# Performance work log

Hardware: AMD Instinct MI355X
Metric: run time of the kernel (lower is better)

Reference implementation:

```python
import jax, jax.numpy as jnp
import numpy as np

STATE_LEN = 512
DIM_KEY = 128


def _rope(t, offset):
    # t: (b, h, s, d) -> rotate-half RoPE with given position offset
    b, h, s, d = t.shape
    inv_freq = 1.0 / (10000.0 ** (jnp.arange(0, d, 2, dtype=jnp.float32) / d))
    pos = jnp.arange(s, dtype=jnp.float32) + offset
    ang = pos[:, None] * inv_freq[None, :]            # (s, d/2)
    cos = jnp.concatenate([jnp.cos(ang), jnp.cos(ang)], axis=-1)  # (s, d)
    sin = jnp.concatenate([jnp.sin(ang), jnp.sin(ang)], axis=-1)
    t1, t2 = t[..., : d // 2], t[..., d // 2 :]
    rot = jnp.concatenate([-t2, t1], axis=-1)
    return t * cos + rot * sin


def _proj(x, w):
    # StackedLinear: mixes heads and features. x: (b,h,s,d), w: (h_in,h_out,d_in,d_out)
    return jnp.einsum('bhsd,hgde->bgse', x, w)


def setup_inputs() -> dict:
    key = jax.random.key(0)
    ks = jax.random.split(key, 10)
    x = jax.random.normal(ks[0], (2, 8, 3072, 128), dtype=jnp.float32)
    wshape = (8, 8, 128, 128)
    names = ['Wq', 'Wk', 'Wv', 'Wqs', 'Wks', 'Wvs', 'Wqe', 'Wke', 'Wve']
    inp = {'x': x}
    for i, n in enumerate(names):
        inp[n] = jax.random.normal(ks[i + 1], wshape, dtype=jnp.float32) * 0.02
    inp['offset'] = 0
    return inp


def reference(x, Wq, Wk, Wv, Wqs, Wks, Wvs, Wqe, Wke, Wve, offset):
    # extract_state: front state, middle, end state along seq axis
    xs = x[:, :, :STATE_LEN]
    xm = x[:, :, STATE_LEN:-STATE_LEN]
    xe = x[:, :, -STATE_LEN:]

    q = jnp.concatenate([_proj(xs, Wqs), _proj(xm, Wq), _proj(xe, Wqe)], axis=2)
    k = jnp.concatenate([_proj(xs, Wks), _proj(xm, Wk), _proj(xe, Wke)], axis=2)
    v = jnp.concatenate([_proj(xs, Wvs), _proj(xm, Wv), _proj(xe, Wve)], axis=2)

    q = _rope(q, offset)
    k = _rope(k, offset)

    scores = jnp.einsum('bhqd,bhkd->bhqk', q, k) / (DIM_KEY ** 0.5)
    s = scores.shape[-1]
    mask = jnp.tril(jnp.ones((s, s), dtype=bool))
    scores = jnp.where(mask[None, None], scores, -jnp.inf)
    att = jax.nn.softmax(scores, axis=-1)
    return jnp.einsum('bhqk,bhkd->bhqd', att, v)
```

## Files before the change

### kernel.cpp

```cpp
#include <hip/hip_runtime.h>
#include <hip/hip_bf16.h>
#include <stdint.h>


typedef __bf16   bf16x8 __attribute__((ext_vector_type(8)));
typedef float    f32x4  __attribute__((ext_vector_type(4)));
typedef uint32_t u32x4  __attribute__((ext_vector_type(4)));
typedef uint16_t u16x4  __attribute__((ext_vector_type(4)));

struct f2 { float c, s; };

#define SEQ   3072
#define NFRQ  64

static __device__ __forceinline__ uint16_t f2bf(float f) {
  union { float f; uint32_t u; } v; v.f = f;
  uint32_t r = (v.u + 0x7FFFu + ((v.u >> 16) & 1u)) >> 16;
  return (uint16_t)r;
}
static __device__ __forceinline__ float bf2f(uint16_t u) {
  union { uint32_t u; float f; } v; v.u = ((uint32_t)u) << 16;
  return v.f;
}
static __device__ __forceinline__ bf16x8 ldlds(const uint16_t* base, int byteoff) {
  u32x4 t = *reinterpret_cast<const u32x4*>(reinterpret_cast<const char*>(base) + byteoff);
  return __builtin_bit_cast(bf16x8, t);
}
static __device__ __forceinline__ bf16x8 ldglb(const uint16_t* p) {
  u32x4 t = *reinterpret_cast<const u32x4*>(p);
  return __builtin_bit_cast(bf16x8, t);
}

__global__ __launch_bounds__(256) void rope_table_kernel(f2* tab, const int* offp) {
  int i = blockIdx.x * 256 + threadIdx.x;
  if (i >= SEQ * NFRQ) return;
  int s = i >> 6, f = i & 63;
  float pos = (float)(s + offp[0]);
  float inv = powf(10000.0f, -(float)(2 * f) / 128.0f);
  float ang = pos * inv;
  tab[i].c = cosf(ang);
  tab[i].s = sinf(ang);
}

__global__ __launch_bounds__(256) void conv_x_kernel(const float* __restrict__ x,
                                                     uint16_t* __restrict__ xb) {
  int i = blockIdx.x * 256 + threadIdx.x;
  int d4 = i & 31;
  int t  = i >> 5;
  int s  = t % 3072;
  int bh = t / 3072;
  int h  = bh & 7, b = bh >> 3;
  f32x4 v = reinterpret_cast<const f32x4*>(x)[i];
  u16x4 o = { f2bf(v[0]), f2bf(v[1]), f2bf(v[2]), f2bf(v[3]) };
  size_t dst = ((size_t)(b * 3072 + s)) * 1024 + h * 128 + d4 * 4;
  *reinterpret_cast<u16x4*>(xb + dst) = o;
}

__global__ __launch_bounds__(256) void trans_w_kernel(
    const float* W0, const float* W1, const float* W2,
    const float* W3, const float* W4, const float* W5,
    const float* W6, const float* W7, const float* W8,
    uint16_t* __restrict__ Wt) {
  const float* Wall[9] = { W0, W1, W2, W3, W4, W5, W6, W7, W8 };
  int blk  = blockIdx.x;
  int widx = blk >> 6;
  int hg   = blk & 63;
  int h = hg >> 3, g = hg & 7;
  int qkv = widx / 3, seg = widx % 3;
  int sel = (seg == 0) ? (3 + qkv) : ((seg == 1) ? qkv : (6 + qkv));
  const float* src = Wall[sel] + (((size_t)h * 8 + g) * 128) * 128;
  uint16_t* dst = Wt + (((size_t)widx * 8 + g) * 128) * 1024 + h * 128;

  __shared__ uint16_t T[128 * 129];
  int tid = threadIdx.x;
  #pragma unroll
  for (int i = 0; i < 16; ++i) {
    int idx = tid + i * 256;
    int d = idx >> 5, e4 = idx & 31;
    f32x4 v = *reinterpret_cast<const f32x4*>(src + d * 128 + e4 * 4);
    int base = d * 129 + e4 * 4;
    T[base + 0] = f2bf(v[0]); T[base + 1] = f2bf(v[1]);
    T[base + 2] = f2bf(v[2]); T[base + 3] = f2bf(v[3]);
  }
  __syncthreads();
  #pragma unroll
  for (int i = 0; i < 8; ++i) {
    int idx = tid + i * 256;
    int e = idx >> 4, c = idx & 15, d0 = c * 8;
    uint32_t w0 = (uint32_t)T[(d0 + 0) * 129 + e] | ((uint32_t)T[(d0 + 1) * 129 + e] << 16);
    uint32_t w1 = (uint32_t)T[(d0 + 2) * 129 + e] | ((uint32_t)T[(d0 + 3) * 129 + e] << 16);
    uint32_t w2 = (uint32_t)T[(d0 + 4) * 129 + e] | ((uint32_t)T[(d0 + 5) * 129 + e] << 16);
    uint32_t w3 = (uint32_t)T[(d0 + 6) * 129 + e] | ((uint32_t)T[(d0 + 7) * 129 + e] << 16);
    u32x4 o = { w0, w1, w2, w3 };
    *reinterpret_cast<u32x4*>(dst + (size_t)e * 1024 + d0) = o;
  }
}

__global__ __launch_bounds__(256) void proj_kernel(
    const uint16_t* __restrict__ xb, const uint16_t* __restrict__ Wt,
    const f2* __restrict__ rtab,
    uint16_t* __restrict__ qb, uint16_t* __restrict__ kb,
    uint16_t* __restrict__ vtb) {
  const int bid = blockIdx.x;
  const int qkv = bid / 384;
  const int rem = bid % 384;
  const int mt  = rem >> 3;
  const int g   = rem & 7;
  const int R0  = mt * 128;
  const int b   = R0 / 3072;
  const int s0  = R0 % 3072;
  const int seg = (s0 < 512) ? 0 : ((s0 < 2560) ? 1 : 2);

  const uint16_t* Ag = xb + (size_t)R0 * 1024;
  const uint16_t* Bg = Wt + (((size_t)(qkv * 3 + seg) * 8 + g) << 17);

  __shared__ __align__(16) uint16_t Al[128 * 64];
  __shared__ __align__(16) uint16_t Bl[128 * 64];

  const int tid  = threadIdx.x;
  const int lane = tid & 63;
  const int w    = tid >> 6;
  const int l15  = lane & 15;
  const int l4   = lane >> 4;

  f32x4 acc[2][8];
  #pragma unroll
  for (int rf = 0; rf < 2; ++rf)
    #pragma unroll
    for (int nf = 0; nf < 8; ++nf) acc[rf][nf] = (f32x4){0.f, 0.f, 0.f, 0.f};

  for (int k0 = 0; k0 < 1024; k0 += 64) {
    #pragma unroll
    for (int i = 0; i < 4; ++i) {
      int idx = tid + i * 256;
      int r = idx >> 3, c8 = idx & 7;
      int off = (r * 128 + c8 * 16) ^ ((r & 7) << 4);
      u32x4 va = *reinterpret_cast<const u32x4*>(Ag + (size_t)r * 1024 + k0 + c8 * 8);
      *reinterpret_cast<u32x4*>(reinterpret_cast<char*>(Al) + off) = va;
      u32x4 vb = *reinterpret_cast<const u32x4*>(Bg + (size_t)r * 1024 + k0 + c8 * 8);
      *reinterpret_cast<u32x4*>(reinterpret_cast<char*>(Bl) + off) = vb;
    }
    __syncthreads();

    bf16x8 af[2][2];
    #pragma unroll
    for (int rf = 0; rf < 2; ++rf)
      #pragma unroll
      for (int kf = 0; kf < 2; ++kf) {
        int row = w * 32 + rf * 16 + l15;
        af[rf][kf] = ldlds(Al, (row * 128 + kf * 64 + l4 * 16) ^ ((row & 7) << 4));
      }
    #pragma unroll
    for (int nf = 0; nf < 8; ++nf) {
      int row = nf * 16 + l15;
      bf16x8 b0 = ldlds(Bl, (row * 128 + 0  + l4 * 16) ^ ((row & 7) << 4));
      bf16x8 b1 = ldlds(Bl, (row * 128 + 64 + l4 * 16) ^ ((row & 7) << 4));
      #pragma unroll
      for (int rf = 0; rf < 2; ++rf) {
        acc[rf][nf] = __builtin_amdgcn_mfma_f32_16x16x32_bf16(af[rf][0], b0, acc[rf][nf], 0, 0, 0);
        acc[rf][nf] = __builtin_amdgcn_mfma_f32_16x16x32_bf16(af[rf][1], b1, acc[rf][nf], 0, 0, 0);
      }
    }
    __syncthreads();
  }

  const int bg = b * 8 + g;
  if (qkv == 2) {
    #pragma unroll
    for (int rf = 0; rf < 2; ++rf)
      #pragma unroll
      for (int nf = 0; nf < 8; ++nf) {
        int e = nf * 16 + l15;
        int s = s0 + w * 32 + rf * 16 + l4 * 4;
        u16x4 pk = { f2bf(acc[rf][nf][0]), f2bf(acc[rf][nf][1]),
                     f2bf(acc[rf][nf][2]), f2bf(acc[rf][nf][3]) };
        *reinterpret_cast<u16x4*>(vtb + ((size_t)bg * 128 + e) * 3072 + s) = pk;
      }
  } else {
    uint16_t* outp = (qkv == 0) ? qb : kb;
    const float scl = (qkv == 0) ? 0.08838834764831845f : 1.0f;
    #pragma unroll
    for (int rf = 0; rf < 2; ++rf)
      #pragma unroll
      for (int j = 0; j < 4; ++j) {
        int s = s0 + w * 32 + rf * 16 + l4 * 4 + j;
        size_t rowb = ((size_t)bg * 3072 + s) * 128;
        #pragma unroll
        for (int nf = 0; nf < 4; ++nf) {
          int f = nf * 16 + l15;
          f2 cs = rtab[s * 64 + f];
          float q1 = acc[rf][nf][j], q2 = acc[rf][nf + 4][j];
          outp[rowb + f]      = f2bf((q1 * cs.c - q2 * cs.s) * scl);
          outp[rowb + 64 + f] = f2bf((q2 * cs.c + q1 * cs.s) * scl);
        }
      }
  }
}

__global__ __launch_bounds__(256) void attn_kernel(
    const uint16_t* __restrict__ qb, const uint16_t* __restrict__ kb,
    const uint16_t* __restrict__ vtb, float* __restrict__ out,
    float* __restrict__ opart, float* __restrict__ lsum) {
  const int bid = blockIdx.x;
  const int bg  = bid & 15;
  const int idx = 47 - (bid >> 4);
  int qt, c;
  if (idx < 8)       { qt = idx;               c = 0; }
  else if (idx < 24) { qt = 8 + ((idx - 8) >> 1);  c = (idx - 8) & 1; }
  else               { int r = idx - 24; qt = 16 + r / 3; c = r - (qt - 16) * 3; }
  const int q0  = qt * 128;
  const int nkv = 2 * qt + 2;
  const int t0  = c * 16;
  const int t1  = (t0 + 16 < nkv) ? (t0 + 16) : nkv;

  const uint16_t* Qp = qb  + (size_t)bg * 3072 * 128;
  const uint16_t* Kp = kb  + (size_t)bg * 3072 * 128;
  const uint16_t* Vp = vtb + (size_t)bg * 128 * 3072;

  __shared__ __align__(16) uint16_t Kl[2][64 * 128];
  __shared__ __align__(16) uint16_t Vl[128 * 64];
  __shared__ __align__(16) uint16_t Pl[128 * 64];

  const int tid  = threadIdx.x;
  const int lane = tid & 63;
  const int w    = tid >> 6;
  const int l15  = lane & 15;
  const int l4   = lane >> 4;
  const int wrow = w * 32;

  bf16x8 aq[2][4];
  #pragma unroll
  for (int rf = 0; rf < 2; ++rf)
    #pragma unroll
    for (int kf = 0; kf < 4; ++kf) {
      int row = q0 + wrow + rf * 16 + l15;
      aq[rf][kf] = ldglb(Qp + (size_t)row * 128 + kf * 32 + l4 * 8);
    }

  f32x4 acc[2][8];
  #pragma unroll
  for (int rf = 0; rf < 2; ++rf)
    #pragma unroll
    for (int ef = 0; ef < 8; ++ef) acc[rf][ef] = (f32x4){0.f, 0.f, 0.f, 0.f};
  float lrow[2][4];
  #pragma unroll
  for (int rf = 0; rf < 2; ++rf)
    #pragma unroll
    for (int j = 0; j < 4; ++j) lrow[rf][j] = 0.f;

  u32x4 kreg[4], vreg[4];
  {
    const int k0 = t0 * 64;
    #pragma unroll
    for (int i = 0; i < 4; ++i) {
      int id2 = tid + i * 256;
      kreg[i] = *reinterpret_cast<const u32x4*>(Kp + (size_t)(k0 + (id2 >> 4)) * 128 + (id2 & 15) * 8);
      vreg[i] = *reinterpret_cast<const u32x4*>(Vp + (size_t)(id2 >> 3) * 3072 + k0 + (id2 & 7) * 8);
    }
    #pragma unroll
    for (int i = 0; i < 4; ++i) {
      int id2 = tid + i * 256;
      int r = id2 >> 4, cc = id2 & 15;
      *reinterpret_cast<u32x4*>(reinterpret_cast<char*>(Kl[0]) +
          ((r * 256 + cc * 16) ^ ((r & 7) << 4))) = kreg[i];
      int e = id2 >> 3, c8 = id2 & 7;
      *reinterpret_cast<u32x4*>(reinterpret_cast<char*>(Vl) +
          ((e * 128 + c8 * 16) ^ ((e & 7) << 4))) = vreg[i];
    }
  }

  for (int t = t0; t < t1; ++t) {
    const int lt = (t - t0) & 1;
    __syncthreads();
    const bool more = (t + 1 < t1);
    if (more) {
      const int k0n = (t + 1) * 64;
      #pragma unroll
      for (int i = 0; i < 4; ++i) {
        int id2 = tid + i * 256;
        kreg[i] = *reinterpret_cast<const u32x4*>(Kp + (size_t)(k0n + (id2 >> 4)) * 128 + (id2 & 15) * 8);
        vreg[i] = *reinterpret_cast<const u32x4*>(Vp + (size_t)(id2 >> 3) * 3072 + k0n + (id2 & 7) * 8);
      }
    }

    const int k0 = t * 64;
    if (k0 <= q0 + wrow + 31) {
      f32x4 sc[2][4];
      #pragma unroll
      for (int rf = 0; rf < 2; ++rf)
        #pragma unroll
        for (int nf = 0; nf < 4; ++nf) sc[rf][nf] = (f32x4){0.f, 0.f, 0.f, 0.f};

      #pragma unroll
      for (int nf = 0; nf < 4; ++nf) {
        int row = nf * 16 + l15;
        #pragma unroll
        for (int kf = 0; kf < 4; ++kf) {
          bf16x8 bk = ldlds(Kl[lt], (row * 256 + kf * 64 + l4 * 16) ^ ((row & 7) << 4));
          #pragma unroll
          for (int rf = 0; rf < 2; ++rf)
            sc[rf][nf] = __builtin_amdgcn_mfma_f32_16x16x32_bf16(aq[rf][kf], bk, sc[rf][nf], 0, 0, 0);
        }
      }

      if (k0 + 63 > q0 + wrow) {
        #pragma unroll
        for (int rf = 0; rf < 2; ++rf)
          #pragma unroll
          for (int nf = 0; nf < 4; ++nf)
            #pragma unroll
            for (int j = 0; j < 4; ++j) {
              int qr = q0 + wrow + rf * 16 + l4 * 4 + j;
              int kc = k0 + nf * 16 + l15;
              if (kc > qr) sc[rf][nf][j] = -1.0e30f;
            }
      }

      #pragma unroll
      for (int rf = 0; rf < 2; ++rf)
        #pragma unroll
        for (int nf = 0; nf < 4; ++nf)
          #pragma unroll
          for (int j = 0; j < 4; ++j) {
            float p  = __expf(sc[rf][nf][j] - 3.0f);
            uint16_t pb = f2bf(p);
            lrow[rf][j] += bf2f(pb);
            int qr = wrow + rf * 16 + l4 * 4 + j;
            int kc = nf * 16 + l15;
            *reinterpret_cast<uint16_t*>(reinterpret_cast<char*>(Pl) +
                ((qr * 128 + kc * 2) ^ ((qr & 7) << 4))) = pb;
          }

      bf16x8 ap[2][2];
      #pragma unroll
      for (int rf = 0; rf < 2; ++rf)
        #pragma unroll
        for (int kf = 0; kf < 2; ++kf) {
          int row = wrow + rf * 16 + l15;
          ap[rf][kf] = ldlds(Pl, (row * 128 + kf * 64 + l4 * 16) ^ ((row & 7) << 4));
        }
      #pragma unroll
      for (int ef = 0; ef < 8; ++ef) {
        int e = ef * 16 + l15;
        bf16x8 bv0 = ldlds(Vl, (e * 128 + 0  + l4 * 16) ^ ((e & 7) << 4));
        bf16x8 bv1 = ldlds(Vl, (e * 128 + 64 + l4 * 16) ^ ((e & 7) << 4));
        #pragma unroll
        for (int rf = 0; rf < 2; ++rf) {
          acc[rf][ef] = __builtin_amdgcn_mfma_f32_16x16x32_bf16(ap[rf][0], bv0, acc[rf][ef], 0, 0, 0);
          acc[rf][ef] = __builtin_amdgcn_mfma_f32_16x16x32_bf16(ap[rf][1], bv1, acc[rf][ef], 0, 0, 0);
        }
      }
    }

    if (more) {
      #pragma unroll
      for (int i = 0; i < 4; ++i) {
        int id2 = tid + i * 256;
        int r = id2 >> 4, cc = id2 & 15;
        *reinterpret_cast<u32x4*>(reinterpret_cast<char*>(Kl[lt ^ 1]) +
            ((r * 256 + cc * 16) ^ ((r & 7) << 4))) = kreg[i];
      }
      __syncthreads();
      #pragma unroll
      for (int i = 0; i < 4; ++i) {
        int id2 = tid + i * 256;
        int e = id2 >> 3, c8 = id2 & 7;
        *reinterpret_cast<u32x4*>(reinterpret_cast<char*>(Vl) +
            ((e * 128 + c8 * 16) ^ ((e & 7) << 4))) = vreg[i];
      }
    }
  }

  const int chunkid = bg * 48 + idx;
  float* obase;
  if (c == 0) {
    obase = out + ((size_t)bg * 3072 + q0) * 128;
  } else {
    int slot = bg * 24 + ((qt < 16) ? (qt - 8) : (8 + (qt - 16) * 2 + (c - 1)));
    obase = opart + (size_t)slot * 16384;
  }
  #pragma unroll
  for (int rf = 0; rf < 2; ++rf)
    #pragma unroll
    for (int j = 0; j < 4; ++j) {
      float ps = lrow[rf][j];
      #pragma unroll
      for (int off = 1; off < 16; off <<= 1)
        ps += __shfl_xor(ps, off);
      int rl = wrow + rf * 16 + l4 * 4 + j;
      if (l15 == 0)
        lsum[(size_t)chunkid * 128 + rl] = ps;
      #pragma unroll
      for (int ef = 0; ef < 8; ++ef)
        obase[(size_t)rl * 128 + ef * 16 + l15] = acc[rf][ef][j];
    }
}

__global__ __launch_bounds__(256) void combine_kernel(
    float* __restrict__ out, const float* __restrict__ opart,
    const float* __restrict__ lsum) {
  const int bid = blockIdx.x;
  const int bg = bid / 24, qt = bid % 24;
  const int nc = (qt < 8) ? 1 : ((qt < 16) ? 2 : 3);
  const int idx0 = (qt < 8) ? qt : ((qt < 16) ? (8 + (qt - 8) * 2) : (24 + (qt - 16) * 3));
  const int t = threadIdx.x;
  const int r = t >> 1, half = t & 1;

  const float* lb = lsum + (size_t)(bg * 48 + idx0) * 128 + r;
  float l = lb[0];
  if (nc > 1) l += lb[128];
  if (nc > 2) l += lb[256];
  float inv = 1.0f / l;

  float* orow = out + ((size_t)bg * 3072 + qt * 128 + r) * 128 + half * 64;
  f32x4 a[16];
  #pragma unroll
  for (int v = 0; v < 16; ++v)
    a[v] = reinterpret_cast<const f32x4*>(orow)[v];
  if (nc > 1) {
    int slot = bg * 24 + ((qt < 16) ? (qt - 8) : (8 + (qt - 16) * 2));
    const float* p = opart + (size_t)slot * 16384 + r * 128 + half * 64;
    #pragma unroll
    for (int v = 0; v < 16; ++v) a[v] += reinterpret_cast<const f32x4*>(p)[v];
  }
  if (nc > 2) {
    int slot = bg * 24 + (8 + (qt - 16) * 2 + 1);
    const float* p = opart + (size_t)slot * 16384 + r * 128 + half * 64;
    #pragma unroll
    for (int v = 0; v < 16; ++v) a[v] += reinterpret_cast<const f32x4*>(p)[v];
  }
  #pragma unroll
  for (int v = 0; v < 16; ++v)
    reinterpret_cast<f32x4*>(orow)[v] = a[v] * inv;
}

extern "C" void kernel_launch(void* const* d_in, const int* in_sizes, int n_in,
                              void* d_out, int out_size, void* d_ws, size_t ws_size,
                              hipStream_t stream) {
  const float* x = (const float*)d_in[0];
  const float* W[9];
  for (int i = 0; i < 9; ++i) W[i] = (const float*)d_in[1 + i];
  const int* offset = (const int*)d_in[10];
  float* out = (float*)d_out;

  char* ws = (char*)d_ws;
  f2*       rtab  = (f2*)(ws + 0);
  uint16_t* xb    = (uint16_t*)(ws + 1572864);
  uint16_t* Wt    = (uint16_t*)(ws + 14155776);
  uint16_t* qb    = (uint16_t*)(ws + 33030144);
  uint16_t* kb    = (uint16_t*)(ws + 45613056);
  uint16_t* vtb   = (uint16_t*)(ws + 58195968);
  float*    opart = (float*)(ws + 0);
  float*    lsum  = (float*)(ws + 25165824);

  hipLaunchKernelGGL(rope_table_kernel, dim3(768),  dim3(256), 0, stream, rtab, offset);
  hipLaunchKernelGGL(conv_x_kernel,     dim3(6144), dim3(256), 0, stream, x, xb);
  hipLaunchKernelGGL(trans_w_kernel,    dim3(576),  dim3(256), 0, stream,
                     W[0], W[1], W[2], W[3], W[4], W[5], W[6], W[7], W[8], Wt);
  hipLaunchKernelGGL(proj_kernel,       dim3(1152), dim3(256), 0, stream,
                     xb, Wt, rtab, qb, kb, vtb);
  hipLaunchKernelGGL(attn_kernel,       dim3(768),  dim3(256), 0, stream,
                     qb, kb, vtb, out, opart, lsum);
  hipLaunchKernelGGL(combine_kernel,    dim3(384),  dim3(256), 0, stream,
                     out, opart, lsum);
}
```

Before: 238.8 us.

## Split attention KV range into finer chunks with table-driven scheduling and bf16 partials

Attention work is split into chunks of 8 KV tiles instead of 16, giving 84 chunks per head instead of 48. Blocks are scheduled through lookup tables so the longest query tiles go first. The QK MFMA operands are swapped so each lane holds a query row, which lets P be written to LDS as packed 8-byte stores and shrinks the row-sum reduction. Partial outputs are now stored as bf16, which halves partial-buffer traffic but adds more partials to combine and some precision loss.

```diff
diff --git a/kernel.cpp b/kernel.cpp
--- a/kernel.cpp
+++ b/kernel.cpp
@@ -6,12 +6,26 @@
 typedef __bf16   bf16x8 __attribute__((ext_vector_type(8)));
 typedef float    f32x4  __attribute__((ext_vector_type(4)));
 typedef uint32_t u32x4  __attribute__((ext_vector_type(4)));
+typedef uint32_t u32x2  __attribute__((ext_vector_type(2)));
 typedef uint16_t u16x4  __attribute__((ext_vector_type(4)));
 
 struct f2 { float c, s; };
 
 #define SEQ   3072
 #define NFRQ  64
+
+__device__ const uint8_t TQT[84] = {
+  3,4,5,6, 7,7,8,8,9,9,10,10, 11,11,11,12,12,12,13,13,13,14,14,14,
+  15,15,15,15,16,16,16,16,17,17,17,17,18,18,18,18,
+  19,19,19,19,19,20,20,20,20,20,21,21,21,21,21,22,22,22,22,22,
+  23,23,23,23,23,23, 2,6,10,14,18,22, 1,5,9,13,17,21, 0,4,8,12,16,20 };
+__device__ const uint8_t TC[84] = {
+  0,0,0,0, 0,1,0,1,0,1,0,1, 0,1,2,0,1,2,0,1,2,0,1,2,
+  0,1,2,3,0,1,2,3,0,1,2,3,0,1,2,3,
+  0,1,2,3,4,0,1,2,3,4,0,1,2,3,4,0,1,2,3,4,
+  0,1,2,3,4,5, 0,1,2,3,4,5, 0,1,2,3,4,5, 0,1,2,3,4,5 };
+__device__ const uint8_t PT[24]  = {0,0,0,0,0,1,2,3,4,6,8,10,12,15,18,21,24,28,32,36,40,45,50,55};
+__device__ const uint8_t CCT[24] = {0,1,2,3,4,6,8,10,12,15,18,21,24,28,32,36,40,45,50,55,60,66,72,78};
 
 static __device__ __forceinline__ uint16_t f2bf(float f) {
   union { float f; uint32_t u; } v; v.f = f;
@@ -200,18 +214,16 @@
 __global__ __launch_bounds__(256) void attn_kernel(
     const uint16_t* __restrict__ qb, const uint16_t* __restrict__ kb,
     const uint16_t* __restrict__ vtb, float* __restrict__ out,
-    float* __restrict__ opart, float* __restrict__ lsum) {
+    uint16_t* __restrict__ opart, float* __restrict__ lsum) {
   const int bid = blockIdx.x;
   const int bg  = bid & 15;
-  const int idx = 47 - (bid >> 4);
-  int qt, c;
-  if (idx < 8)       { qt = idx;               c = 0; }
-  else if (idx < 24) { qt = 8 + ((idx - 8) >> 1);  c = (idx - 8) & 1; }
-  else               { int r = idx - 24; qt = 16 + r / 3; c = r - (qt - 16) * 3; }
+  const int idx = bid >> 4;
+  const int qt  = TQT[idx];
+  const int c   = TC[idx];
   const int q0  = qt * 128;
   const int nkv = 2 * qt + 2;
-  const int t0  = c * 16;
-  const int t1  = (t0 + 16 < nkv) ? (t0 + 16) : nkv;
+  const int t0  = c * 8;
+  const int t1  = (t0 + 8 < nkv) ? (t0 + 8) : nkv;
 
   const uint16_t* Qp = qb  + (size_t)bg * 3072 * 128;
   const uint16_t* Kp = kb  + (size_t)bg * 3072 * 128;
@@ -242,11 +254,7 @@
   for (int rf = 0; rf < 2; ++rf)
     #pragma unroll
     for (int ef = 0; ef < 8; ++ef) acc[rf][ef] = (f32x4){0.f, 0.f, 0.f, 0.f};
-  float lrow[2][4];
-  #pragma unroll
-  for (int rf = 0; rf < 2; ++rf)
-    #pragma unroll
-    for (int j = 0; j < 4; ++j) lrow[rf][j] = 0.f;
+  float lrow[2] = {0.f, 0.f};
 
   u32x4 kreg[4], vreg[4];
   {
@@ -299,7 +307,7 @@
           bf16x8 bk = ldlds(Kl[lt], (row * 256 + kf * 64 + l4 * 16) ^ ((row & 7) << 4));
           #pragma unroll
           for (int rf = 0; rf < 2; ++rf)
-            sc[rf][nf] = __builtin_amdgcn_mfma_f32_16x16x32_bf16(aq[rf][kf], bk, sc[rf][nf], 0, 0, 0);
+            sc[rf][nf] = __builtin_amdgcn_mfma_f32_16x16x32_bf16(bk, aq[rf][kf], sc[rf][nf], 0, 0, 0);
         }
       }
 
@@ -310,26 +318,30 @@
           for (int nf = 0; nf < 4; ++nf)
             #pragma unroll
             for (int j = 0; j < 4; ++j) {
-              int qr = q0 + wrow + rf * 16 + l4 * 4 + j;
-              int kc = k0 + nf * 16 + l15;
+              int qr = q0 + wrow + rf * 16 + l15;
+              int kc = k0 + nf * 16 + l4 * 4 + j;
               if (kc > qr) sc[rf][nf][j] = -1.0e30f;
             }
       }
 
       #pragma unroll
-      for (int rf = 0; rf < 2; ++rf)
-        #pragma unroll
-        for (int nf = 0; nf < 4; ++nf)
-          #pragma unroll
-          for (int j = 0; j < 4; ++j) {
-            float p  = __expf(sc[rf][nf][j] - 3.0f);
-            uint16_t pb = f2bf(p);
-            lrow[rf][j] += bf2f(pb);
-            int qr = wrow + rf * 16 + l4 * 4 + j;
-            int kc = nf * 16 + l15;
-            *reinterpret_cast<uint16_t*>(reinterpret_cast<char*>(Pl) +
-                ((qr * 128 + kc * 2) ^ ((qr & 7) << 4))) = pb;
-          }
+      for (int rf = 0; rf < 2; ++rf) {
+        int qr = wrow + rf * 16 + l15;
+        int rowb = qr * 128;
+        int swz = (qr & 7) << 4;
+        #pragma unroll
+        for (int nf = 0; nf < 4; ++nf) {
+          uint16_t pb0 = f2bf(__expf(sc[rf][nf][0] - 3.0f));
+          uint16_t pb1 = f2bf(__expf(sc[rf][nf][1] - 3.0f));
+          uint16_t pb2 = f2bf(__expf(sc[rf][nf][2] - 3.0f));
+          uint16_t pb3 = f2bf(__expf(sc[rf][nf][3] - 3.0f));
+          lrow[rf] += bf2f(pb0) + bf2f(pb1) + bf2f(pb2) + bf2f(pb3);
+          u32x2 dw = { (uint32_t)pb0 | ((uint32_t)pb1 << 16),
+                       (uint32_t)pb2 | ((uint32_t)pb3 << 16) };
+          *reinterpret_cast<u32x2*>(reinterpret_cast<char*>(Pl) +
+              ((rowb + nf * 32 + l4 * 8) ^ swz)) = dw;
+        }
+      }
 
       bf16x8 ap[2][2];
       #pragma unroll
@@ -371,45 +383,55 @@
     }
   }
 
-  const int chunkid = bg * 48 + idx;
-  float* obase;
+  const int lidx = bg * 84 + CCT[qt] + c;
+  #pragma unroll
+  for (int rf = 0; rf < 2; ++rf) {
+    float ps = lrow[rf];
+    ps += __shfl_xor(ps, 16);
+    ps += __shfl_xor(ps, 32);
+    if (l4 == 0)
+      lsum[(size_t)lidx * 128 + wrow + rf * 16 + l15] = ps;
+  }
   if (c == 0) {
-    obase = out + ((size_t)bg * 3072 + q0) * 128;
+    float* obase = out + ((size_t)bg * 3072 + q0) * 128;
+    #pragma unroll
+    for (int rf = 0; rf < 2; ++rf)
+      #pragma unroll
+      for (int j = 0; j < 4; ++j) {
+        int rl = wrow + rf * 16 + l4 * 4 + j;
+        #pragma unroll
+        for (int ef = 0; ef < 8; ++ef)
+          obase[(size_t)rl * 128 + ef * 16 + l15] = acc[rf][ef][j];
+      }
   } else {
-    int slot = bg * 24 + ((qt < 16) ? (qt - 8) : (8 + (qt - 16) * 2 + (c - 1)));
-    obase = opart + (size_t)slot * 16384;
-  }
-  #pragma unroll
-  for (int rf = 0; rf < 2; ++rf)
-    #pragma unroll
-    for (int j = 0; j < 4; ++j) {
-      float ps = lrow[rf][j];
-      #pragma unroll
-      for (int off = 1; off < 16; off <<= 1)
-        ps += __shfl_xor(ps, off);
-      int rl = wrow + rf * 16 + l4 * 4 + j;
-      if (l15 == 0)
-        lsum[(size_t)chunkid * 128 + rl] = ps;
-      #pragma unroll
-      for (int ef = 0; ef < 8; ++ef)
-        obase[(size_t)rl * 128 + ef * 16 + l15] = acc[rf][ef][j];
-    }
+    int slot = bg * 60 + PT[qt] + (c - 1);
+    uint16_t* pbase = opart + (size_t)slot * 16384;
+    #pragma unroll
+    for (int rf = 0; rf < 2; ++rf)
+      #pragma unroll
+      for (int j = 0; j < 4; ++j) {
+        int rl = wrow + rf * 16 + l4 * 4 + j;
+        #pragma unroll
+        for (int ef = 0; ef < 8; ++ef)
+          pbase[rl * 128 + ef * 16 + l15] = f2bf(acc[rf][ef][j]);
+      }
+  }
 }
 
 __global__ __launch_bounds__(256) void combine_kernel(
-    float* __restrict__ out, const float* __restrict__ opart,
+    float* __restrict__ out, const uint16_t* __restrict__ opart,
     const float* __restrict__ lsum) {
   const int bid = blockIdx.x;
   const int bg = bid / 24, qt = bid % 24;
-  const int nc = (qt < 8) ? 1 : ((qt < 16) ? 2 : 3);
-  const int idx0 = (qt < 8) ? qt : ((qt < 16) ? (8 + (qt - 8) * 2) : (24 + (qt - 16) * 3));
+  const int nc = (qt >> 2) + 1;
+  const int lbase = bg * 84 + CCT[qt];
+  const int pbase = bg * 60 + PT[qt];
   const int t = threadIdx.x;
   const int r = t >> 1, half = t & 1;
 
-  const float* lb = lsum + (size_t)(bg * 48 + idx0) * 128 + r;
-  float l = lb[0];
-  if (nc > 1) l += lb[128];
-  if (nc > 2) l += lb[256];
+  float l = 0.f;
+  for (int c2 = 0; c2 < nc; ++c2)
+    l += lsum[(size_t)(lbase + c2) * 128 + r];
   float inv = 1.0f / l;
 
   float* orow = out + ((size_t)bg * 3072 + qt * 128 + r) * 128 + half * 64;
@@ -417,17 +439,13 @@
   #pragma unroll
   for (int v = 0; v < 16; ++v)
     a[v] = reinterpret_cast<const f32x4*>(orow)[v];
-  if (nc > 1) {
-    int slot = bg * 24 + ((qt < 16) ? (qt - 8) : (8 + (qt - 16) * 2));
-    const float* p = opart + (size_t)slot * 16384 + r * 128 + half * 64;
-    #pragma unroll
-    for (int v = 0; v < 16; ++v) a[v] += reinterpret_cast<const f32x4*>(p)[v];
-  }
-  if (nc > 2) {
-    int slot = bg * 24 + (8 + (qt - 16) * 2 + 1);
-    const float* p = opart + (size_t)slot * 16384 + r * 128 + half * 64;
-    #pragma unroll
-    for (int v = 0; v < 16; ++v) a[v] += reinterpret_cast<const f32x4*>(p)[v];
+  for (int c2 = 1; c2 < nc; ++c2) {
+    const uint16_t* p = opart + (size_t)(pbase + c2 - 1) * 16384 + r * 128 + half * 64;
+    #pragma unroll
+    for (int v = 0; v < 16; ++v) {
+      u16x4 pk = reinterpret_cast<const u16x4*>(p)[v];
+      a[v] += (f32x4){ bf2f(pk[0]), bf2f(pk[1]), bf2f(pk[2]), bf2f(pk[3]) };
+    }
   }
   #pragma unroll
   for (int v = 0; v < 16; ++v)
@@ -450,8 +468,8 @@
   uint16_t* qb    = (uint16_t*)(ws + 33030144);
   uint16_t* kb    = (uint16_t*)(ws + 45613056);
   uint16_t* vtb   = (uint16_t*)(ws + 58195968);
-  float*    opart = (float*)(ws + 0);
-  float*    lsum  = (float*)(ws + 25165824);
+  uint16_t* opart = (uint16_t*)(ws + 0);
+  float*    lsum  = (float*)(ws + 31457280);
 
   hipLaunchKernelGGL(rope_table_kernel, dim3(768),  dim3(256), 0, stream, rtab, offset);
   hipLaunchKernelGGL(conv_x_kernel,     dim3(6144), dim3(256), 0, stream, x, xb);
@@ -459,7 +477,7 @@
                      W[0], W[1], W[2], W[3], W[4], W[5], W[6], W[7], W[8], Wt);
   hipLaunchKernelGGL(proj_kernel,       dim3(1152), dim3(256), 0, stream,
                      xb, Wt, rtab, qb, kb, vtb);
-  hipLaunchKernelGGL(attn_kernel,       dim3(768),  dim3(256), 0, stream,
+  hipLaunchKernelGGL(attn_kernel,       dim3(1344), dim3(256), 0, stream,
                      qb, kb, vtb, out, opart, lsum);
   hipLaunchKernelGGL(combine_kernel,    dim3(384),  dim3(256), 0, stream,
                      out, opart, lsum);
```

Measured after the change: 229.6 us. 1.04x faster.
